# Kernel tuning notes

Measured on AMD Instinct MI355X. Metric: run time of the kernel, lower is better.

## Reference

```python
import jax, jax.numpy as jnp
import numpy as np
import math

B, H, S, D, P = 1, 8, 512, 64, 32  # batch, heads, seq, d_k, proj_dim


def setup_inputs() -> dict:
    key = jax.random.key(0)
    ks = jax.random.split(key, 9)
    mu = math.log(math.sqrt(2.0 / D))  # PositiveLinear raw init mean

    def raw(k):
        return mu + 0.2 * jax.random.normal(k, (D, D), jnp.float32)

    return dict(
        q=jax.random.normal(ks[0], (B, H, S, D), jnp.float32),
        k=jax.random.normal(ks[1], (B, H, S, D), jnp.float32),
        v=jax.random.normal(ks[2], (B, H, S, D), jnp.float32),
        sq_raw1=raw(ks[3]), sq_b1=jnp.zeros((D,), jnp.float32),
        sq_raw2=raw(ks[4]), sq_b2=jnp.zeros((D,), jnp.float32),
        sk_raw1=raw(ks[5]), sk_b1=jnp.zeros((D,), jnp.float32),
        sk_raw2=raw(ks[6]), sk_b2=jnp.zeros((D,), jnp.float32),
        Wh=jax.random.normal(ks[7], (P, D), jnp.float32) / jnp.sqrt(jnp.float32(D)),
        Wv=jax.random.normal(ks[8], (P, D), jnp.float32) / jnp.sqrt(jnp.float32(D)),
    )


def _icnn(x, r1, b1, r2, b2):
    # Input-convex net: positive weights via softplus, softplus activations.
    z = jax.nn.softplus(x @ jax.nn.softplus(r1).T + b1)
    z = jax.nn.softplus(z @ jax.nn.softplus(r2).T + b2)
    return z.sum(-1)  # scalar convex score per token: [B,H,S]


def reference(q, k, v, sq_raw1, sq_b1, sq_raw2, sq_b2,
              sk_raw1, sk_b1, sk_raw2, sk_b2, Wh, Wv):
    f_q = _icnn(q, sq_raw1, sq_b1, sq_raw2, sq_b2)  # [B,H,S]
    g_k = _icnn(k, sk_raw1, sk_b1, sk_raw2, sk_b2)  # [B,H,S]
    phi_q = jnp.exp(q @ Wh.T)  # [B,H,S,P]
    phi_k = jnp.exp(k @ Wh.T)  # [B,H,S,P]
    scores = jnp.einsum('bhsr,bhtr->bhst', phi_q, phi_k)  # [B,H,S,S], strictly positive
    s_ij = f_q[..., :, None] + g_k[..., None, :] + jnp.log(scores)  # [B,H,S,S]
    u = v @ Wv.T  # [B,H,S,P] (index t)
    Sz = s_ij.shape[-1]
    # y[bhsp] = logsumexp_t(s_ij[bhst] + u[bhtp]) - log S, computed without the 5D tensor:
    m1 = jax.lax.stop_gradient(jnp.max(s_ij, axis=-1, keepdims=True))  # [B,H,S,1]
    m2 = jax.lax.stop_gradient(jnp.max(u, axis=2, keepdims=True))      # [B,H,1,P]
    acc = jnp.einsum('bhst,bhtp->bhsp', jnp.exp(s_ij - m1), jnp.exp(u - m2))
    y = jnp.log(acc) + m1 + m2 - jnp.log(jnp.float32(Sz))
    return y  # [B,H,S,P]
```

## Files before the change

kernel.cpp:

```cpp
#include <hip/hip_runtime.h>
#include <math.h>

#define HH 8
#define SS 512
#define DD 64
#define PP 32


__device__ __forceinline__ float softplusf(float x) {
    if (x > 20.f) return x;
    return log1pf(__expf(x));
}

__global__ __launch_bounds__(256) void csm_token4(
    const float* __restrict__ q, const float* __restrict__ k, const float* __restrict__ v,
    const float* __restrict__ sq_raw1, const float* __restrict__ sq_b1,
    const float* __restrict__ sq_raw2, const float* __restrict__ sq_b2,
    const float* __restrict__ sk_raw1, const float* __restrict__ sk_b1,
    const float* __restrict__ sk_raw2, const float* __restrict__ sk_b2,
    const float* __restrict__ Wh, const float* __restrict__ Wv,
    float* __restrict__ fq, float* __restrict__ gk, float* __restrict__ gkpart,
    float* __restrict__ phiq, float* __restrict__ phik, float* __restrict__ uexp)
{
    __shared__ float xs[32 * 68];
    __shared__ float wb[64 * 68];
    __shared__ float wh[32 * 68];
    __shared__ float part[32 * 17];
    __shared__ float bb1[64], bb2[64];

    const int bx   = blockIdx.x;
    const int role = bx >> 7;
    const int sub  = bx & 127;
    const int g0   = sub * 32;
    const int tid  = threadIdx.x;
    const int tr = tid >> 4, tc = tid & 15;
    const int m0 = tr * 2, n0 = tc * 4, p0 = tc * 2;

    const float* xin = (role == 0) ? q : (role == 1) ? k : v;

    const float4* xsrc = (const float4*)(xin + g0 * 64);
    #pragma unroll
    for (int c = 0; c < 2; ++c) {
        int idx4 = tid + c * 256;
        int t = idx4 >> 4, ic = (idx4 & 15) * 4;
        *(float4*)&xs[t * 68 + ic] = xsrc[idx4];
    }
    const float4* whsrc = (const float4*)((role == 2) ? Wv : Wh);
    #pragma unroll
    for (int c = 0; c < 2; ++c) {
        int idx4 = tid + c * 256;
        int r = idx4 >> 4, i0 = (idx4 & 15) * 4;
        *(float4*)&wh[r * 68 + i0] = whsrc[idx4];
    }

    float4 rw2[4];
    if (role < 2) {
        const float4* r1src = (const float4*)(role == 0 ? sq_raw1 : sk_raw1);
        const float4* r2src = (const float4*)(role == 0 ? sq_raw2 : sk_raw2);
        #pragma unroll
        for (int c = 0; c < 4; ++c) {
            int idx4 = tid + c * 256;
            int j = idx4 >> 4, i0 = (idx4 & 15) * 4;
            float4 w = r1src[idx4];
            w.x = softplusf(w.x); w.y = softplusf(w.y);
            w.z = softplusf(w.z); w.w = softplusf(w.w);
            *(float4*)&wb[j * 68 + i0] = w;
            rw2[c] = r2src[idx4];
        }
        if (tid < 64)       bb1[tid]      = (role == 0 ? sq_b1 : sk_b1)[tid];
        else if (tid < 128) bb2[tid - 64] = (role == 0 ? sq_b2 : sk_b2)[tid - 64];
    }
    __syncthreads();

    if (role == 2) {
        float acc[2][2] = {{0.f,0.f},{0.f,0.f}};
        #pragma unroll
        for (int kc = 0; kc < 16; ++kc) {
            const int i0 = kc * 4;
            float4 xv[2], hw[2];
            xv[0] = *(const float4*)&xs[(m0 + 0) * 68 + i0];
            xv[1] = *(const float4*)&xs[(m0 + 1) * 68 + i0];
            hw[0] = *(const float4*)&wh[(p0 + 0) * 68 + i0];
            hw[1] = *(const float4*)&wh[(p0 + 1) * 68 + i0];
            #pragma unroll
            for (int mm = 0; mm < 2; ++mm) {
                const float* xa = (const float*)&xv[mm];
                const float* h0 = (const float*)&hw[0];
                const float* h1 = (const float*)&hw[1];
                #pragma unroll
                for (int kk = 0; kk < 4; ++kk) {
                    acc[mm][0] += xa[kk] * h0[kk];
                    acc[mm][1] += xa[kk] * h1[kk];
                }
            }
        }
        #pragma unroll
        for (int mm = 0; mm < 2; ++mm) {
            float2 o; o.x = __expf(acc[mm][0]); o.y = __expf(acc[mm][1]);
            *(float2*)&uexp[(g0 + m0 + mm) * 32 + p0] = o;
        }
        return;
    }

    float acc[2][4], accp[2][2];
    #pragma unroll
    for (int mm = 0; mm < 2; ++mm) {
        #pragma unroll
        for (int j = 0; j < 4; ++j) acc[mm][j] = bb1[n0 + j];
        accp[mm][0] = 0.f; accp[mm][1] = 0.f;
    }
    #pragma unroll
    for (int kc = 0; kc < 16; ++kc) {
        const int i0 = kc * 4;
        float4 xv[2], wn[4], hw[2];
        xv[0] = *(const float4*)&xs[(m0 + 0) * 68 + i0];
        xv[1] = *(const float4*)&xs[(m0 + 1) * 68 + i0];
        #pragma unroll
        for (int jj = 0; jj < 4; ++jj)
            wn[jj] = *(const float4*)&wb[(n0 + jj) * 68 + i0];
        hw[0] = *(const float4*)&wh[(p0 + 0) * 68 + i0];
        hw[1] = *(const float4*)&wh[(p0 + 1) * 68 + i0];
        #pragma unroll
        for (int mm = 0; mm < 2; ++mm) {
            const float* xa = (const float*)&xv[mm];
            const float* h0 = (const float*)&hw[0];
            const float* h1 = (const float*)&hw[1];
            #pragma unroll
            for (int kk = 0; kk < 4; ++kk) {
                const float xmk = xa[kk];
                acc[mm][0] += xmk * ((const float*)&wn[0])[kk];
                acc[mm][1] += xmk * ((const float*)&wn[1])[kk];
                acc[mm][2] += xmk * ((const float*)&wn[2])[kk];
                acc[mm][3] += xmk * ((const float*)&wn[3])[kk];
                accp[mm][0] += xmk * h0[kk];
                accp[mm][1] += xmk * h1[kk];
            }
        }
    }
    float* phiout = (role == 0) ? phiq : phik;
    #pragma unroll
    for (int mm = 0; mm < 2; ++mm) {
        float2 o; o.x = __expf(accp[mm][0]); o.y = __expf(accp[mm][1]);
        *(float2*)&phiout[(g0 + m0 + mm) * 32 + p0] = o;
    }
    float z1v[2][4];
    #pragma unroll
    for (int mm = 0; mm < 2; ++mm)
        #pragma unroll
        for (int j = 0; j < 4; ++j) z1v[mm][j] = softplusf(acc[mm][j]);
    __syncthreads();
    #pragma unroll
    for (int mm = 0; mm < 2; ++mm)
        *(float4*)&xs[(m0 + mm) * 68 + n0] = *(float4*)&z1v[mm][0];
    #pragma unroll
    for (int c = 0; c < 4; ++c) {
        int idx4 = tid + c * 256;
        int j = idx4 >> 4, i0 = (idx4 & 15) * 4;
        float4 w = rw2[c];
        w.x = softplusf(w.x); w.y = softplusf(w.y);
        w.z = softplusf(w.z); w.w = softplusf(w.w);
        *(float4*)&wb[j * 68 + i0] = w;
    }
    __syncthreads();

    float acc2[2][4];
    #pragma unroll
    for (int mm = 0; mm < 2; ++mm)
        #pragma unroll
        for (int j = 0; j < 4; ++j) acc2[mm][j] = bb2[n0 + j];
    #pragma unroll
    for (int kc = 0; kc < 16; ++kc) {
        const int i0 = kc * 4;
        float4 xv[2], wn[4];
        xv[0] = *(const float4*)&xs[(m0 + 0) * 68 + i0];
        xv[1] = *(const float4*)&xs[(m0 + 1) * 68 + i0];
        #pragma unroll
        for (int jj = 0; jj < 4; ++jj)
            wn[jj] = *(const float4*)&wb[(n0 + jj) * 68 + i0];
        #pragma unroll
        for (int mm = 0; mm < 2; ++mm) {
            const float* xa = (const float*)&xv[mm];
            #pragma unroll
            for (int kk = 0; kk < 4; ++kk) {
                const float xmk = xa[kk];
                acc2[mm][0] += xmk * ((const float*)&wn[0])[kk];
                acc2[mm][1] += xmk * ((const float*)&wn[1])[kk];
                acc2[mm][2] += xmk * ((const float*)&wn[2])[kk];
                acc2[mm][3] += xmk * ((const float*)&wn[3])[kk];
            }
        }
    }
    #pragma unroll
    for (int mm = 0; mm < 2; ++mm) {
        float s = softplusf(acc2[mm][0]) + softplusf(acc2[mm][1])
                + softplusf(acc2[mm][2]) + softplusf(acc2[mm][3]);
        part[(m0 + mm) * 17 + tc] = s;
    }
    __syncthreads();
    if (tid < 32) {
        float s = 0.f;
        #pragma unroll
        for (int c = 0; c < 16; ++c) s += part[tid * 17 + c];
        if (role == 0) fq[g0 + tid] = s;
        else           gk[g0 + tid] = s;
        if (role == 1) {
            float mx = s;
            #pragma unroll
            for (int off = 16; off >= 1; off >>= 1)
                mx = fmaxf(mx, __shfl_xor(mx, off, 32));
            if (tid == 0) gkpart[sub] = mx;
        }
    }
}

__global__ __launch_bounds__(256) void csm_reduceM(
    const float* __restrict__ gk, const float* __restrict__ gkpart,
    const float* __restrict__ phik, const float* __restrict__ uexp,
    float* __restrict__ Mpart, float* __restrict__ Gbuf)
{
    __shared__ float wls[128];
    __shared__ float pk[128 * 36];
    __shared__ float wu[128 * 36];

    const int h     = blockIdx.x >> 2;
    const int chunk = blockIdx.x & 3;
    const int tid   = threadIdx.x;
    const int t0    = chunk * 128;

    float G = gkpart[h * 16];
    #pragma unroll
    for (int i = 1; i < 16; ++i) G = fmaxf(G, gkpart[h * 16 + i]);
    if (chunk == 0 && tid == 0) Gbuf[h] = G;

    if (tid < 128) wls[tid] = __expf(gk[h * SS + t0 + tid] - G);
    __syncthreads();

    const float4* psrc = (const float4*)(phik + (h * SS + t0) * PP);
    const float4* usrc = (const float4*)(uexp + (h * SS + t0) * PP);
    #pragma unroll
    for (int c = 0; c < 4; ++c) {
        int idx4 = tid + c * 256;
        int t = idx4 >> 3, pc = (idx4 & 7) * 4;
        *(float4*)&pk[t * 36 + pc] = psrc[idx4];
        float4 uv = usrc[idx4];
        float w = wls[t];
        uv.x *= w; uv.y *= w; uv.z *= w; uv.w *= w;
        *(float4*)&wu[t * 36 + pc] = uv;
    }
    __syncthreads();

    const int r0 = (tid >> 5) * 4, p = tid & 31;
    float macc[4] = {0.f, 0.f, 0.f, 0.f};
    for (int t = 0; t < 128; ++t) {
        const float wup = wu[t * 36 + p];
        const float4 pv = *(const float4*)&pk[t * 36 + r0];
        macc[0] += pv.x * wup;
        macc[1] += pv.y * wup;
        macc[2] += pv.z * wup;
        macc[3] += pv.w * wup;
    }
    float* mp = Mpart + blockIdx.x * 1024;
    #pragma unroll
    for (int rr = 0; rr < 4; ++rr)
        mp[(r0 + rr) * 32 + p] = macc[rr];
}

__global__ __launch_bounds__(256) void csm_out(
    const float* __restrict__ fq, const float* __restrict__ phiq,
    const float* __restrict__ Mpart, const float* __restrict__ Gbuf,
    float* __restrict__ y)
{
    __shared__ float Ms[32 * 36];
    __shared__ float pqs[8 * 32];
    __shared__ float fqs[8];

    const int bx = blockIdx.x;
    const int s0 = bx * 8;
    const int h  = bx >> 6;
    const int tid = threadIdx.x;

    {
        const int e = tid * 4;
        const float* base = Mpart + h * 4 * 1024 + e;
        float4 a = *(const float4*)(base);
        float4 b = *(const float4*)(base + 1024);
        float4 c = *(const float4*)(base + 2048);
        float4 d = *(const float4*)(base + 3072);
        float4 s;
        s.x = a.x + b.x + c.x + d.x;
        s.y = a.y + b.y + c.y + d.y;
        s.z = a.z + b.z + c.z + d.z;
        s.w = a.w + b.w + c.w + d.w;
        *(float4*)&Ms[(tid >> 3) * 36 + (tid & 7) * 4] = s;
    }
    pqs[tid] = phiq[s0 * 32 + tid];
    if (tid < 8) fqs[tid] = fq[s0 + tid];
    __syncthreads();

    const int si = tid >> 5, p = tid & 31;
    float acc = 0.f;
    #pragma unroll
    for (int rc = 0; rc < 8; ++rc) {
        const float4 pq = *(const float4*)&pqs[si * 32 + rc * 4];
        acc += pq.x * Ms[(rc * 4 + 0) * 36 + p];
        acc += pq.y * Ms[(rc * 4 + 1) * 36 + p];
        acc += pq.z * Ms[(rc * 4 + 2) * 36 + p];
        acc += pq.w * Ms[(rc * 4 + 3) * 36 + p];
    }
    const float LOG_S = 6.2383246250395078f;
    y[(s0 + si) * 32 + p] = __logf(acc) + fqs[si] + Gbuf[h] - LOG_S;
}

extern "C" void kernel_launch(void* const* d_in, const int* in_sizes, int n_in,
                              void* d_out, int out_size, void* d_ws, size_t ws_size,
                              hipStream_t stream) {
    (void)in_sizes; (void)n_in; (void)out_size; (void)ws_size;
    const float* q       = (const float*)d_in[0];
    const float* k       = (const float*)d_in[1];
    const float* v       = (const float*)d_in[2];
    const float* sq_raw1 = (const float*)d_in[3];
    const float* sq_b1   = (const float*)d_in[4];
    const float* sq_raw2 = (const float*)d_in[5];
    const float* sq_b2   = (const float*)d_in[6];
    const float* sk_raw1 = (const float*)d_in[7];
    const float* sk_b1   = (const float*)d_in[8];
    const float* sk_raw2 = (const float*)d_in[9];
    const float* sk_b2   = (const float*)d_in[10];
    const float* Wh      = (const float*)d_in[11];
    const float* Wv      = (const float*)d_in[12];
    float* y = (float*)d_out;

    float* ws     = (float*)d_ws;
    float* fq     = ws;
    float* gk     = ws + 4096;
    float* gkpart = ws + 8192;
    float* Gbuf   = ws + 8320;
    float* phiq   = ws + 8448;
    float* phik   = ws + 139520;
    float* uexp   = ws + 270592;
    float* Mpart  = ws + 401664;

    csm_token4<<<384, 256, 0, stream>>>(q, k, v,
                                        sq_raw1, sq_b1, sq_raw2, sq_b2,
                                        sk_raw1, sk_b1, sk_raw2, sk_b2,
                                        Wh, Wv,
                                        fq, gk, gkpart, phiq, phik, uexp);
    csm_reduceM<<<32, 256, 0, stream>>>(gk, gkpart, phik, uexp, Mpart, Gbuf);
    csm_out<<<512, 256, 0, stream>>>(fq, phiq, Mpart, Gbuf, y);
}
```

Baseline: 110.3 us.

## Transpose weight tiles in shared memory and split M reduction into more blocks

Stores the softplus'd ICNN weights and the projection weights transposed (k-major) in shared memory. Each thread can then read contiguous float4/float2 rows per k-step instead of strided rows per output column, which should cut LDS bank conflicts in the token kernel. Separately, the reduceM kernel now handles 64 tokens per block across 64 blocks instead of 128 tokens across 32, so more CUs work on it, and csm_out sums 8 partials instead of 4. The transposed stores into shared memory are scalar and may conflict, and Mpart doubles in size; the workspace offset must have room for it.

Result: faster. 108.1 us (-2.0%).

```diff
diff --git a/kernel.cpp b/kernel.cpp
--- a/kernel.cpp
+++ b/kernel.cpp
@@ -12,7 +12,7 @@
     return log1pf(__expf(x));
 }
 
-__global__ __launch_bounds__(256) void csm_token4(
+__global__ __launch_bounds__(256) void csm_token5(
     const float* __restrict__ q, const float* __restrict__ k, const float* __restrict__ v,
     const float* __restrict__ sq_raw1, const float* __restrict__ sq_b1,
     const float* __restrict__ sq_raw2, const float* __restrict__ sq_b2,
@@ -24,7 +24,7 @@
 {
     __shared__ float xs[32 * 68];
     __shared__ float wb[64 * 68];
-    __shared__ float wh[32 * 68];
+    __shared__ float wh[64 * 36];
     __shared__ float part[32 * 17];
     __shared__ float bb1[64], bb2[64];
 
@@ -49,10 +49,13 @@
     #pragma unroll
     for (int c = 0; c < 2; ++c) {
         int idx4 = tid + c * 256;
-        int r = idx4 >> 4, i0 = (idx4 & 15) * 4;
-        *(float4*)&wh[r * 68 + i0] = whsrc[idx4];
-    }
-
+        int p = idx4 >> 4, i0 = (idx4 & 15) * 4;
+        float4 w = whsrc[idx4];
+        wh[(i0 + 0) * 36 + p] = w.x;
+        wh[(i0 + 1) * 36 + p] = w.y;
+        wh[(i0 + 2) * 36 + p] = w.z;
+        wh[(i0 + 3) * 36 + p] = w.w;
+    }
     float4 rw2[4];
     if (role < 2) {
         const float4* r1src = (const float4*)(role == 0 ? sq_raw1 : sk_raw1);
@@ -62,9 +65,10 @@
             int idx4 = tid + c * 256;
             int j = idx4 >> 4, i0 = (idx4 & 15) * 4;
             float4 w = r1src[idx4];
-            w.x = softplusf(w.x); w.y = softplusf(w.y);
-            w.z = softplusf(w.z); w.w = softplusf(w.w);
-            *(float4*)&wb[j * 68 + i0] = w;
+            wb[(i0 + 0) * 68 + j] = softplusf(w.x);
+            wb[(i0 + 1) * 68 + j] = softplusf(w.y);
+            wb[(i0 + 2) * 68 + j] = softplusf(w.z);
+            wb[(i0 + 3) * 68 + j] = softplusf(w.w);
             rw2[c] = r2src[idx4];
         }
         if (tid < 64)       bb1[tid]      = (role == 0 ? sq_b1 : sk_b1)[tid];
@@ -77,20 +81,18 @@
         #pragma unroll
         for (int kc = 0; kc < 16; ++kc) {
             const int i0 = kc * 4;
-            float4 xv[2], hw[2];
+            float4 xv[2]; float2 hv[4];
             xv[0] = *(const float4*)&xs[(m0 + 0) * 68 + i0];
             xv[1] = *(const float4*)&xs[(m0 + 1) * 68 + i0];
-            hw[0] = *(const float4*)&wh[(p0 + 0) * 68 + i0];
-            hw[1] = *(const float4*)&wh[(p0 + 1) * 68 + i0];
+            #pragma unroll
+            for (int kk = 0; kk < 4; ++kk) hv[kk] = *(const float2*)&wh[(i0 + kk) * 36 + p0];
             #pragma unroll
             for (int mm = 0; mm < 2; ++mm) {
                 const float* xa = (const float*)&xv[mm];
-                const float* h0 = (const float*)&hw[0];
-                const float* h1 = (const float*)&hw[1];
                 #pragma unroll
                 for (int kk = 0; kk < 4; ++kk) {
-                    acc[mm][0] += xa[kk] * h0[kk];
-                    acc[mm][1] += xa[kk] * h1[kk];
+                    acc[mm][0] += xa[kk] * hv[kk].x;
+                    acc[mm][1] += xa[kk] * hv[kk].y;
                 }
             }
         }
@@ -112,28 +114,27 @@
     #pragma unroll
     for (int kc = 0; kc < 16; ++kc) {
         const int i0 = kc * 4;
-        float4 xv[2], wn[4], hw[2];
+        float4 xv[2], wv[4]; float2 hv[4];
         xv[0] = *(const float4*)&xs[(m0 + 0) * 68 + i0];
         xv[1] = *(const float4*)&xs[(m0 + 1) * 68 + i0];
         #pragma unroll
-        for (int jj = 0; jj < 4; ++jj)
-            wn[jj] = *(const float4*)&wb[(n0 + jj) * 68 + i0];
-        hw[0] = *(const float4*)&wh[(p0 + 0) * 68 + i0];
-        hw[1] = *(const float4*)&wh[(p0 + 1) * 68 + i0];
+        for (int kk = 0; kk < 4; ++kk) {
+            wv[kk] = *(const float4*)&wb[(i0 + kk) * 68 + n0];
+            hv[kk] = *(const float2*)&wh[(i0 + kk) * 36 + p0];
+        }
         #pragma unroll
         for (int mm = 0; mm < 2; ++mm) {
             const float* xa = (const float*)&xv[mm];
-            const float* h0 = (const float*)&hw[0];
-            const float* h1 = (const float*)&hw[1];
             #pragma unroll
             for (int kk = 0; kk < 4; ++kk) {
                 const float xmk = xa[kk];
-                acc[mm][0] += xmk * ((const float*)&wn[0])[kk];
-                acc[mm][1] += xmk * ((const float*)&wn[1])[kk];
-                acc[mm][2] += xmk * ((const float*)&wn[2])[kk];
-                acc[mm][3] += xmk * ((const float*)&wn[3])[kk];
-                accp[mm][0] += xmk * h0[kk];
-                accp[mm][1] += xmk * h1[kk];
+                const float* wa = (const float*)&wv[kk];
+                acc[mm][0] += xmk * wa[0];
+                acc[mm][1] += xmk * wa[1];
+                acc[mm][2] += xmk * wa[2];
+                acc[mm][3] += xmk * wa[3];
+                accp[mm][0] += xmk * hv[kk].x;
+                accp[mm][1] += xmk * hv[kk].y;
             }
         }
     }
@@ -157,9 +158,10 @@
         int idx4 = tid + c * 256;
         int j = idx4 >> 4, i0 = (idx4 & 15) * 4;
         float4 w = rw2[c];
-        w.x = softplusf(w.x); w.y = softplusf(w.y);
-        w.z = softplusf(w.z); w.w = softplusf(w.w);
-        *(float4*)&wb[j * 68 + i0] = w;
+        wb[(i0 + 0) * 68 + j] = softplusf(w.x);
+        wb[(i0 + 1) * 68 + j] = softplusf(w.y);
+        wb[(i0 + 2) * 68 + j] = softplusf(w.z);
+        wb[(i0 + 3) * 68 + j] = softplusf(w.w);
     }
     __syncthreads();
 
@@ -171,22 +173,22 @@
     #pragma unroll
     for (int kc = 0; kc < 16; ++kc) {
         const int i0 = kc * 4;
-        float4 xv[2], wn[4];
+        float4 xv[2], wv[4];
         xv[0] = *(const float4*)&xs[(m0 + 0) * 68 + i0];
         xv[1] = *(const float4*)&xs[(m0 + 1) * 68 + i0];
         #pragma unroll
-        for (int jj = 0; jj < 4; ++jj)
-            wn[jj] = *(const float4*)&wb[(n0 + jj) * 68 + i0];
+        for (int kk = 0; kk < 4; ++kk) wv[kk] = *(const float4*)&wb[(i0 + kk) * 68 + n0];
         #pragma unroll
         for (int mm = 0; mm < 2; ++mm) {
             const float* xa = (const float*)&xv[mm];
             #pragma unroll
             for (int kk = 0; kk < 4; ++kk) {
                 const float xmk = xa[kk];
-                acc2[mm][0] += xmk * ((const float*)&wn[0])[kk];
-                acc2[mm][1] += xmk * ((const float*)&wn[1])[kk];
-                acc2[mm][2] += xmk * ((const float*)&wn[2])[kk];
-                acc2[mm][3] += xmk * ((const float*)&wn[3])[kk];
+                const float* wa = (const float*)&wv[kk];
+                acc2[mm][0] += xmk * wa[0];
+                acc2[mm][1] += xmk * wa[1];
+                acc2[mm][2] += xmk * wa[2];
+                acc2[mm][3] += xmk * wa[3];
             }
         }
     }
@@ -218,27 +220,27 @@
     const float* __restrict__ phik, const float* __restrict__ uexp,
     float* __restrict__ Mpart, float* __restrict__ Gbuf)
 {
-    __shared__ float wls[128];
-    __shared__ float pk[128 * 36];
-    __shared__ float wu[128 * 36];
-
-    const int h     = blockIdx.x >> 2;
-    const int chunk = blockIdx.x & 3;
+    __shared__ float wls[64];
+    __shared__ float pk[64 * 36];
+    __shared__ float wu[64 * 36];
+
+    const int h     = blockIdx.x >> 3;
+    const int chunk = blockIdx.x & 7;
     const int tid   = threadIdx.x;
-    const int t0    = chunk * 128;
+    const int t0    = chunk * 64;
 
     float G = gkpart[h * 16];
     #pragma unroll
     for (int i = 1; i < 16; ++i) G = fmaxf(G, gkpart[h * 16 + i]);
     if (chunk == 0 && tid == 0) Gbuf[h] = G;
 
-    if (tid < 128) wls[tid] = __expf(gk[h * SS + t0 + tid] - G);
+    if (tid < 64) wls[tid] = __expf(gk[h * SS + t0 + tid] - G);
     __syncthreads();
 
     const float4* psrc = (const float4*)(phik + (h * SS + t0) * PP);
     const float4* usrc = (const float4*)(uexp + (h * SS + t0) * PP);
     #pragma unroll
-    for (int c = 0; c < 4; ++c) {
+    for (int c = 0; c < 2; ++c) {
         int idx4 = tid + c * 256;
         int t = idx4 >> 3, pc = (idx4 & 7) * 4;
         *(float4*)&pk[t * 36 + pc] = psrc[idx4];
@@ -251,7 +253,7 @@
 
     const int r0 = (tid >> 5) * 4, p = tid & 31;
     float macc[4] = {0.f, 0.f, 0.f, 0.f};
-    for (int t = 0; t < 128; ++t) {
+    for (int t = 0; t < 64; ++t) {
         const float wup = wu[t * 36 + p];
         const float4 pv = *(const float4*)&pk[t * 36 + r0];
         macc[0] += pv.x * wup;
@@ -281,16 +283,13 @@
 
     {
         const int e = tid * 4;
-        const float* base = Mpart + h * 4 * 1024 + e;
-        float4 a = *(const float4*)(base);
-        float4 b = *(const float4*)(base + 1024);
-        float4 c = *(const float4*)(base + 2048);
-        float4 d = *(const float4*)(base + 3072);
-        float4 s;
-        s.x = a.x + b.x + c.x + d.x;
-        s.y = a.y + b.y + c.y + d.y;
-        s.z = a.z + b.z + c.z + d.z;
-        s.w = a.w + b.w + c.w + d.w;
+        const float* base = Mpart + h * 8 * 1024 + e;
+        float4 s = *(const float4*)(base);
+        #pragma unroll
+        for (int c = 1; c < 8; ++c) {
+            float4 a = *(const float4*)(base + c * 1024);
+            s.x += a.x; s.y += a.y; s.z += a.z; s.w += a.w;
+        }
         *(float4*)&Ms[(tid >> 3) * 36 + (tid & 7) * 4] = s;
     }
     pqs[tid] = phiq[s0 * 32 + tid];
@@ -340,11 +339,11 @@
     float* uexp   = ws + 270592;
     float* Mpart  = ws + 401664;
 
-    csm_token4<<<384, 256, 0, stream>>>(q, k, v,
+    csm_token5<<<384, 256, 0, stream>>>(q, k, v,
                                         sq_raw1, sq_b1, sq_raw2, sq_b2,
                                         sk_raw1, sk_b1, sk_raw2, sk_b2,
                                         Wh, Wv,
                                         fq, gk, gkpart, phiq, phik, uexp);
-    csm_reduceM<<<32, 256, 0, stream>>>(gk, gkpart, phik, uexp, Mpart, Gbuf);
+    csm_reduceM<<<64, 256, 0, stream>>>(gk, gkpart, phik, uexp, Mpart, Gbuf);
     csm_out<<<512, 256, 0, stream>>>(fq, phiq, Mpart, Gbuf, y);
 }
```
